# Kernel tuning notes

Hardware: AMD Instinct MI355X
Metric: run time of the kernel (lower is better)

The kernel has to match this reference:

```python
import jax, jax.numpy as jnp
import numpy as np

RC, RMIN = 6.0, 0.5
BETA, M1, M2 = 12, 24, 6
B, N, NT, MN = 4, 1024, 2, 128
K = NT * MN
NFEAT = M1 * M2


def _cheby(x, order):
    # Chebyshev polynomials T_0..T_{order-1} via recurrence, stacked on last axis
    Ts = [jnp.ones_like(x), x]
    for _ in range(order - 2):
        Ts.append(2.0 * x * Ts[-1] - Ts[-2])
    return jnp.stack(Ts[:order], axis=-1)


def _feat_fn(rxyz, valid, ti_map, c_param, scale):
    # rxyz: (B,N,K,3) neighbor displacement vectors; valid: (B,N,K) 0/1 float
    b, n, k, _ = rxyz.shape
    r = jnp.sqrt(jnp.sum(rxyz * rxyz, axis=-1) + 1e-12)          # (B,N,K)
    u = jnp.clip((r - RMIN) / (RC - RMIN), 0.0, 1.0)
    fc = 0.5 * (jnp.cos(jnp.pi * u) + 1.0) * valid                # smooth cutoff
    x = 2.0 * (r - RMIN) / (RC - RMIN) - 1.0
    T = _cheby(x, BETA).reshape(b, n, NT, MN, BETA)               # group slots by neighbor type
    c_i = c_param[ti_map]                                         # (N, NT, M1, BETA) gather by center type
    s = jnp.einsum('bntmk,ntfk->bntmf', T, c_i).reshape(b, n, k, M1)
    s = s * fc[..., None]                                         # (B,N,K,M1)
    inv_r = valid / r
    sr = jnp.concatenate([valid[..., None], rxyz * inv_r[..., None]], axis=-1)  # (B,N,K,4)
    R = jnp.einsum('bnkf,bnkc->bnfc', s, sr) / MN                 # (B,N,M1,4)
    feat = jnp.einsum('bnfc,bngc->bnfg', R, R[:, :, :M2]).reshape(b, n, NFEAT)
    return feat * scale


def _ei_fn(feat, ti_map, W0, b0, W1, b1, W2, b2, ener_shift):
    # evaluate all per-type fitting nets, then select by atom type
    h = jnp.tanh(jnp.einsum('bnf,tfh->bnth', feat, W0) + b0)
    h2 = jnp.tanh(jnp.einsum('bnth,thg->bntg', h, W1) + b1) + h   # resnet skip
    E = jnp.einsum('bnth,th->bnt', h2, W2) + b2 + ener_shift      # (B,N,T)
    idx = jnp.broadcast_to(ti_map[None, :, None], (E.shape[0], E.shape[1], 1))
    return jnp.take_along_axis(E, idx, axis=2)[..., 0]            # (B,N)


def setup_inputs() -> dict:
    key = jax.random.key(0)
    ks = jax.random.split(key, 16)
    num_neigh = jax.random.randint(ks[0], (B, N, NT), MN // 2, MN + 1)
    slot = jnp.arange(MN)
    vmask = slot[None, None, None, :] < num_neigh[..., None]      # (B,N,NT,MN)
    ln = jax.random.randint(ks[1], (B, N, NT, MN), 0, N)
    list_neigh = jnp.where(vmask, ln, -1)
    r = jax.random.uniform(ks[2], (B, N, K), minval=RMIN + 0.2, maxval=RC - 0.1)
    d = jax.random.normal(ks[3], (B, N, K, 3))
    d = d / jnp.linalg.norm(d, axis=-1, keepdims=True)
    rxyz = d * r[..., None]
    vm = vmask.reshape(B, N, K).astype(jnp.float32)
    ImageDR = jnp.concatenate([r[..., None], rxyz], axis=-1) * vm[..., None]
    return {
        'list_neigh': list_neigh,
        'Imagetype_map': jax.random.randint(ks[4], (N,), 0, NT),
        'atom_type': jnp.arange(NT),
        'ImageDR': ImageDR.astype(jnp.float32),
        'num_neigh': num_neigh,
        'nghost': 0,
        'c_param': jax.random.normal(ks[5], (NT, NT, M1, BETA), jnp.float32) * 0.3,
        'scale': jax.random.uniform(ks[6], (NFEAT,), jnp.float32, 0.5, 1.5),
        'W0': jax.random.normal(ks[7], (NT, NFEAT, 128), jnp.float32) * 0.08,
        'b0': jnp.zeros((NT, 128), jnp.float32),
        'W1': jax.random.normal(ks[8], (NT, 128, 128), jnp.float32) * 0.08,
        'b1': jnp.zeros((NT, 128), jnp.float32),
        'W2': jax.random.normal(ks[9], (NT, 128), jnp.float32) * 0.08,
        'b2': jnp.zeros((NT,), jnp.float32),
        'ener_shift': jax.random.normal(ks[10], (NT,), jnp.float32),
    }


def reference(list_neigh, Imagetype_map, atom_type, ImageDR, num_neigh, nghost,
              c_param, scale, W0, b0, W1, b1, W2, b2, ener_shift):
    ln = list_neigh.reshape(B, N, K)
    valid = (ln >= 0).astype(ImageDR.dtype)
    rxyz = ImageDR[..., 1:4]

    def etot(z):
        feat = _feat_fn(z, valid, Imagetype_map, c_param, scale)
        return _ei_fn(feat, Imagetype_map, W0, b0, W1, b1, W2, b2, ener_shift)

    Ei = etot(rxyz)                                               # (B,N)
    Etot = jnp.sum(Ei, axis=1)                                    # (B,)
    g = jax.grad(lambda z: etot(z).sum())(rxyz)                   # dE/dr_ij  (B,N,K,3)

    natom_tot = N + nghost
    Force = jnp.zeros((B, natom_tot, 3), ImageDR.dtype)
    Force = Force.at[:, :N].add(g.sum(axis=2))                    # center-atom contribution
    idx = jnp.where(ln >= 0, ln, natom_tot).reshape(B, N * K)     # invalid -> pad slot

    def scat(i, v):
        buf = jnp.zeros((natom_tot + 1, 3), v.dtype)
        return buf.at[i].add(v)[:natom_tot]

    Force = Force + jax.vmap(scat)(idx, (-g).reshape(B, N * K, 3))  # scatter to neighbors
    Virial = -jnp.einsum('bnkc,bnkd->bcd', rxyz, g).reshape(B, 9)
    return (Etot, Ei, Force, Virial)
```

## Files before the change

kernel.cpp:

```cpp
#include <hip/hip_runtime.h>
#include <math.h>

#define RMINF  0.5f
#define LSPAN  5.5f
constexpr int BETA = 12, M1 = 24, M2 = 6;
constexpr int B_ = 4, N_ = 1024, NT_ = 2, MN_ = 128;
constexpr int K_ = NT_ * MN_;
constexpr int NFEAT = M1 * M2;
constexpr int HID = 128;
constexpr float PI_F = 3.14159265358979323846f;

constexpr int EI_OFF = B_;
constexpr int F_OFF  = B_ + B_ * N_;
constexpr int V_OFF  = F_OFF + B_ * N_ * 3;

constexpr int G_ = 4;
constexpr int NG = B_ * N_ / G_;
constexpr int SL = 8;

constexpr size_t WS_FEAT    = 0;
constexpr size_t WS_R       = (size_t)B_ * N_ * NFEAT;
constexpr size_t WS_VIR     = WS_R + (size_t)B_ * N_ * 96;
constexpr size_t WS_CONTRIB = WS_VIR + (size_t)NG * 9;
constexpr size_t WS_PARTIAL = WS_CONTRIB + (size_t)NG * N_ * 3;


__global__ __launch_bounds__(256) void k1_embed(
    const int*   __restrict__ list_neigh,
    const int*   __restrict__ type_map,
    const float* __restrict__ imagedr,
    const float* __restrict__ c_param,
    const float* __restrict__ scale,
    float* __restrict__ feat_ws,
    float* __restrict__ R_ws)
{
    __shared__ float c_sh[NT_ * M1 * BETA];
    __shared__ float p_sh[K_][13];
    __shared__ float sr_sh[K_][5];
    __shared__ float Mpart[2][96];
    __shared__ float R_sh[96];

    const int tid = threadIdx.x;
    const int bn = blockIdx.x;
    const int n  = bn % N_;
    const int tn = type_map[n];

    for (int i = tid; i < NT_ * M1 * BETA; i += 256)
        c_sh[i] = c_param[tn * (NT_ * M1 * BETA) + i];

    const int k = tid;
    const int lni = list_neigh[(size_t)bn * K_ + k];
    const float valid = (lni >= 0) ? 1.0f : 0.0f;

    const float4 dr4 = reinterpret_cast<const float4*>(imagedr)[(size_t)bn * K_ + k];
    const float rx = dr4.y, ry = dr4.z, rz = dr4.w;
    const float r  = sqrtf(rx*rx + ry*ry + rz*rz + 1e-12f);
    const float uraw = (r - RMINF) / LSPAN;
    const float u  = fminf(fmaxf(uraw, 0.0f), 1.0f);
    const float fc = 0.5f * (cosf(PI_F * u) + 1.0f) * valid;
    const float x  = 2.0f * (r - RMINF) / LSPAN - 1.0f;

    float T[BETA];
    T[0] = 1.0f; T[1] = x;
#pragma unroll
    for (int j = 2; j < BETA; ++j) T[j] = 2.0f * x * T[j-1] - T[j-2];

    const float inv_r = 1.0f / r;
    sr_sh[k][0] = valid;
    sr_sh[k][1] = valid * rx * inv_r;
    sr_sh[k][2] = valid * ry * inv_r;
    sr_sh[k][3] = valid * rz * inv_r;
#pragma unroll
    for (int j = 0; j < BETA; ++j) p_sh[k][j] = fc * T[j];
    __syncthreads();

    if (tid < 192) {
        const int sub = tid / 96, idx = tid % 96;
        const int tk = idx / 48, rem = idx % 48;
        const int j = rem >> 2, cc = rem & 3;
        const int k0 = tk * 128 + sub * 64;
        float a0 = 0.0f, a1 = 0.0f;
        for (int kk = k0; kk < k0 + 64; kk += 2) {
            a0 = fmaf(p_sh[kk][j],   sr_sh[kk][cc],   a0);
            a1 = fmaf(p_sh[kk+1][j], sr_sh[kk+1][cc], a1);
        }
        Mpart[sub][idx] = a0 + a1;
    }
    __syncthreads();

    if (tid < 96) {
        const int f = tid >> 2, cc = tid & 3;
        float acc = 0.0f;
#pragma unroll
        for (int tk = 0; tk < NT_; ++tk) {
#pragma unroll
            for (int j = 0; j < BETA; ++j) {
                const float m = Mpart[0][tk*48 + j*4 + cc] + Mpart[1][tk*48 + j*4 + cc];
                acc = fmaf(c_sh[tk*288 + f*12 + j], m, acc);
            }
        }
        const float v = acc * (1.0f / MN_);
        R_sh[tid] = v;
        R_ws[(size_t)bn * 96 + tid] = v;
    }
    __syncthreads();
    if (tid < NFEAT) {
        const int f = tid / 6, g = tid % 6;
        float acc = 0.0f;
#pragma unroll
        for (int c = 0; c < 4; ++c) acc += R_sh[f * 4 + c] * R_sh[g * 4 + c];
        feat_ws[(size_t)bn * NFEAT + tid] = acc * scale[tid];
    }
}

__global__ __launch_bounds__(256) void k2_mlp(
    const int*   __restrict__ type_map,
    const float* __restrict__ scale,
    const float* __restrict__ W0,
    const float* __restrict__ b0,
    const float* __restrict__ W1,
    const float* __restrict__ b1,
    const float* __restrict__ W2,
    const float* __restrict__ b2,
    const float* __restrict__ eshift,
    const float* __restrict__ feat_ws,
    float* __restrict__ dfeat_ws,
    float* __restrict__ out)
{
    __shared__ float feat_sh[2][4][NFEAT];
    __shared__ float h_sh[2][4][HID];
    __shared__ float dz1_sh[2][4][HID];
    __shared__ float dz0_sh[2][4][HID];
    __shared__ float red[4][4];

    const int tid  = threadIdx.x;
    const int half = tid >> 7;
    const int c    = tid & 127;
    const int lane = tid & 63;
    const int wid  = tid >> 6;
    const int n0 = blockIdx.x * 2;
    const int n_h = n0 + half;
    const int tn = type_map[n_h];

    for (int i = tid; i < 8 * NFEAT; i += 256) {
        const int a = i / NFEAT, f = i % NFEAT;
        const int hh = a >> 2, bb = a & 3;
        feat_sh[hh][bb][f] = feat_ws[((size_t)bb * N_ + n0 + hh) * NFEAT + f];
    }
    __syncthreads();

    float acc[4];
    const float bias0 = b0[tn * HID + c];
#pragma unroll
    for (int b = 0; b < 4; ++b) acc[b] = bias0;
    const float* w0c = W0 + (size_t)tn * NFEAT * HID + c;
#pragma unroll 4
    for (int f = 0; f < NFEAT; ++f) {
        const float w = w0c[(size_t)f * HID];
#pragma unroll
        for (int b = 0; b < 4; ++b) acc[b] = fmaf(feat_sh[half][b][f], w, acc[b]);
    }
    float hv[4];
#pragma unroll
    for (int b = 0; b < 4; ++b) { hv[b] = tanhf(acc[b]); h_sh[half][b][c] = hv[b]; }
    __syncthreads();

    const float bias1 = b1[tn * HID + c];
#pragma unroll
    for (int b = 0; b < 4; ++b) acc[b] = bias1;
    const float* w1c = W1 + (size_t)tn * HID * HID + c;
#pragma unroll 4
    for (int g = 0; g < HID; ++g) {
        const float w = w1c[(size_t)g * HID];
#pragma unroll
        for (int b = 0; b < 4; ++b) acc[b] = fmaf(h_sh[half][b][g], w, acc[b]);
    }
    const float w2c = W2[tn * HID + c];
    float ei[4];
#pragma unroll
    for (int b = 0; b < 4; ++b) {
        const float t1 = tanhf(acc[b]);
        dz1_sh[half][b][c] = w2c * (1.0f - t1 * t1);
        ei[b] = (t1 + hv[b]) * w2c;
    }
#pragma unroll
    for (int b = 0; b < 4; ++b) {
        float v = ei[b];
#pragma unroll
        for (int m = 32; m >= 1; m >>= 1) v += __shfl_xor(v, m);
        if (lane == 0) red[wid][b] = v;
    }
    __syncthreads();
    if (tid < 8) {
        const int hh = tid >> 2, bb = tid & 3;
        const int nn = n0 + hh;
        const int tt = type_map[nn];
        out[EI_OFF + (size_t)bb * N_ + nn] =
            red[hh*2][bb] + red[hh*2+1][bb] + b2[tt] + eshift[tt];
    }

    {
        const float4* w1row = reinterpret_cast<const float4*>(W1 + (size_t)(tn * HID + c) * HID);
        float ar[4];
#pragma unroll
        for (int b = 0; b < 4; ++b) ar[b] = w2c;
#pragma unroll 2
        for (int g4 = 0; g4 < HID / 4; ++g4) {
            const float4 w = w1row[g4];
#pragma unroll
            for (int b = 0; b < 4; ++b) {
                ar[b] += w.x * dz1_sh[half][b][g4*4+0] + w.y * dz1_sh[half][b][g4*4+1]
                       + w.z * dz1_sh[half][b][g4*4+2] + w.w * dz1_sh[half][b][g4*4+3];
            }
        }
#pragma unroll
        for (int b = 0; b < 4; ++b) dz0_sh[half][b][c] = ar[b] * (1.0f - hv[b] * hv[b]);
    }
    __syncthreads();

    for (int f = c; f < NFEAT; f += HID) {
        const float4* w0row = reinterpret_cast<const float4*>(W0 + (size_t)(tn * NFEAT + f) * HID);
        float ar[4] = {0.0f, 0.0f, 0.0f, 0.0f};
#pragma unroll 2
        for (int h4 = 0; h4 < HID / 4; ++h4) {
            const float4 w = w0row[h4];
#pragma unroll
            for (int b = 0; b < 4; ++b) {
                ar[b] += w.x * dz0_sh[half][b][h4*4+0] + w.y * dz0_sh[half][b][h4*4+1]
                       + w.z * dz0_sh[half][b][h4*4+2] + w.w * dz0_sh[half][b][h4*4+3];
            }
        }
        const float sc = scale[f];
#pragma unroll
        for (int b = 0; b < 4; ++b)
            dfeat_ws[((size_t)b * N_ + n_h) * NFEAT + f] = ar[b] * sc;
    }
}

__global__ __launch_bounds__(256) void k3_bwd(
    const int*   __restrict__ list_neigh,
    const int*   __restrict__ type_map,
    const float* __restrict__ imagedr,
    const float* __restrict__ c_param,
    const float* __restrict__ dfeat_ws,
    const float* __restrict__ R_ws,
    float* __restrict__ contrib_ws,
    float* __restrict__ vir_ws)
{
    __shared__ float fcontrib[N_ * 3];
    __shared__ float c_sh[NT_ * M1 * BETA];
    __shared__ float dfeat_sh[NFEAT];
    __shared__ float R_sh[96];
    __shared__ float dR_sh[96];
    __shared__ float A_sh[96];
    __shared__ float red12[12 * 4];

    const int tid  = threadIdx.x;
    const int lane = tid & 63;
    const int wid  = tid >> 6;
    const int g  = blockIdx.x;
    const int tk = tid >> 7;

    for (int i = tid; i < N_ * 3; i += 256) fcontrib[i] = 0.0f;

    float vv0=0.f,vv1=0.f,vv2=0.f,vv3=0.f,vv4=0.f,vv5=0.f,vv6=0.f,vv7=0.f,vv8=0.f;

    for (int aa = 0; aa < G_; ++aa) {
        const int bn = g * G_ + aa;
        const int n  = bn & (N_ - 1);
        const int tn = type_map[n];

        __syncthreads();
        for (int i = tid; i < NT_ * M1 * BETA; i += 256)
            c_sh[i] = c_param[tn * (NT_ * M1 * BETA) + i];
        if (tid < NFEAT) dfeat_sh[tid] = dfeat_ws[(size_t)bn * NFEAT + tid];
        if (tid < 96)    R_sh[tid]     = R_ws[(size_t)bn * 96 + tid];
        __syncthreads();

        if (tid < 96) {
            const int p = tid >> 2, c = tid & 3;
            float acc = 0.0f;
#pragma unroll
            for (int gg = 0; gg < M2; ++gg) acc += dfeat_sh[p * 6 + gg] * R_sh[gg * 4 + c];
            if (p < M2) {
                for (int f = 0; f < M1; ++f) acc += dfeat_sh[f * 6 + p] * R_sh[f * 4 + c];
            }
            dR_sh[p * 4 + c] = acc * (1.0f / MN_);
        }
        __syncthreads();

        if (tid < 96) {
            const int atk = tid / 48, rem = tid % 48;
            const int j = rem >> 2, cc = rem & 3;
            float acc = 0.0f;
#pragma unroll
            for (int f = 0; f < M1; ++f)
                acc = fmaf(c_sh[atk*288 + f*12 + j], dR_sh[f*4 + cc], acc);
            A_sh[tid] = acc;
        }
        __syncthreads();

        const int lni = list_neigh[(size_t)bn * K_ + tid];
        const float valid = (lni >= 0) ? 1.0f : 0.0f;
        const float4 dr4 = reinterpret_cast<const float4*>(imagedr)[(size_t)bn * K_ + tid];
        const float rx = dr4.y, ry = dr4.z, rz = dr4.w;
        const float r  = sqrtf(rx*rx + ry*ry + rz*rz + 1e-12f);
        const float uraw = (r - RMINF) / LSPAN;
        const float u  = fminf(fmaxf(uraw, 0.0f), 1.0f);
        const float fc = 0.5f * (cosf(PI_F * u) + 1.0f) * valid;
        const float x  = 2.0f * (r - RMINF) / LSPAN - 1.0f;

        float T[BETA];
        T[0] = 1.0f; T[1] = x;
#pragma unroll
        for (int j = 2; j < BETA; ++j) T[j] = 2.0f * x * T[j-1] - T[j-2];

        const float inv_r = 1.0f / r;
        const float sr0 = valid;
        const float sr1 = valid * rx * inv_r;
        const float sr2 = valid * ry * inv_r;
        const float sr3 = valid * rz * inv_r;

        const float* Arow = &A_sh[tk * 48];
        float dfc = 0.0f, dx = 0.0f;
        float tA0 = 0.0f, tA1 = 0.0f, tA2 = 0.0f, tA3 = 0.0f;
        float tpm1 = 1.0f, tpm2 = 0.0f;
#pragma unroll
        for (int j = 0; j < BETA; ++j) {
            const float a0 = Arow[j*4+0], a1 = Arow[j*4+1];
            const float a2 = Arow[j*4+2], a3 = Arow[j*4+3];
            const float cjj = a0*sr0 + a1*sr1 + a2*sr2 + a3*sr3;
            dfc = fmaf(T[j], cjj, dfc);
            tA0 = fmaf(T[j], a0, tA0);
            tA1 = fmaf(T[j], a1, tA1);
            tA2 = fmaf(T[j], a2, tA2);
            tA3 = fmaf(T[j], a3, tA3);
            if (j == 1) {
                dx = cjj;
            } else if (j >= 2) {
                const float tp = 2.0f * T[j-1] + 2.0f * x * tpm1 - tpm2;
                dx = fmaf(cjj, tp, dx);
                tpm2 = tpm1; tpm1 = tp;
            }
        }
        const float dsr1 = fc * tA1, dsr2 = fc * tA2, dsr3 = fc * tA3;

        float dfcdr = 0.0f;
        if (uraw > 0.0f && uraw < 1.0f)
            dfcdr = -0.5f * PI_F * sinf(PI_F * u) * valid / LSPAN;
        const float drt = (fc * dx) * (2.0f / LSPAN) + dfc * dfcdr;
        const float Sdot = dsr1 * rx + dsr2 * ry + dsr3 * rz;
        const float common = drt * inv_r - valid * Sdot * inv_r * inv_r * inv_r;
        const float gx = common * rx + valid * dsr1 * inv_r;
        const float gy = common * ry + valid * dsr2 * inv_r;
        const float gz = common * rz + valid * dsr3 * inv_r;

        if (lni >= 0) {
            atomicAdd(&fcontrib[lni * 3 + 0], -gx);
            atomicAdd(&fcontrib[lni * 3 + 1], -gy);
            atomicAdd(&fcontrib[lni * 3 + 2], -gz);
        }

        {
            float s0 = gx, s1 = gy, s2 = gz;
#pragma unroll
            for (int m = 32; m >= 1; m >>= 1) {
                s0 += __shfl_xor(s0, m);
                s1 += __shfl_xor(s1, m);
                s2 += __shfl_xor(s2, m);
            }
            if (lane == 0) {
                red12[0 * 4 + wid] = s0;
                red12[1 * 4 + wid] = s1;
                red12[2 * 4 + wid] = s2;
            }
        }
        __syncthreads();
        if (tid < 3) {
            const float v = red12[tid*4+0] + red12[tid*4+1] + red12[tid*4+2] + red12[tid*4+3];
            atomicAdd(&fcontrib[n * 3 + tid], v);
        }

        vv0 = fmaf(-rx, gx, vv0); vv1 = fmaf(-rx, gy, vv1); vv2 = fmaf(-rx, gz, vv2);
        vv3 = fmaf(-ry, gx, vv3); vv4 = fmaf(-ry, gy, vv4); vv5 = fmaf(-ry, gz, vv5);
        vv6 = fmaf(-rz, gx, vv6); vv7 = fmaf(-rz, gy, vv7); vv8 = fmaf(-rz, gz, vv8);
    }

    {
        float vals[9] = {vv0,vv1,vv2,vv3,vv4,vv5,vv6,vv7,vv8};
        __syncthreads();
#pragma unroll
        for (int i = 0; i < 9; ++i) {
            float v = vals[i];
#pragma unroll
            for (int m = 32; m >= 1; m >>= 1) v += __shfl_xor(v, m);
            if (lane == 0) red12[i * 4 + wid] = v;
        }
        __syncthreads();
        if (tid < 9)
            vir_ws[(size_t)g * 9 + tid] = red12[tid*4+0] + red12[tid*4+1]
                                        + red12[tid*4+2] + red12[tid*4+3];
    }

    __syncthreads();
    {
        float4* dst = reinterpret_cast<float4*>(contrib_ws + (size_t)g * (N_ * 3));
        const float4* src = reinterpret_cast<const float4*>(fcontrib);
        for (int i = tid; i < (N_ * 3) / 4; i += 256) dst[i] = src[i];
    }
}

__global__ __launch_bounds__(256) void k3_reduce(
    const float* __restrict__ contrib_ws,
    float* __restrict__ partial_ws)
{
    const int x  = blockIdx.x;
    const int ch = x % 3;
    const int bb = (x / 3) % B_;
    const int s  = x / (3 * B_);
    const int c4 = ch * 256 + threadIdx.x;
    const int rows = (NG / B_) / SL;
    const int g0 = bb * (NG / B_) + s * rows;

    const float4* src = reinterpret_cast<const float4*>(contrib_ws);
    float4 a0 = {0,0,0,0}, a1 = {0,0,0,0};
    for (int r = 0; r < rows; r += 2) {
        const float4 v0 = src[(size_t)(g0 + r)     * 768 + c4];
        const float4 v1 = src[(size_t)(g0 + r + 1) * 768 + c4];
        a0.x += v0.x; a0.y += v0.y; a0.z += v0.z; a0.w += v0.w;
        a1.x += v1.x; a1.y += v1.y; a1.z += v1.z; a1.w += v1.w;
    }
    const float4 res = {a0.x + a1.x, a0.y + a1.y, a0.z + a1.z, a0.w + a1.w};
    reinterpret_cast<float4*>(partial_ws)[(size_t)(s * B_ + bb) * 768 + c4] = res;
}

__global__ __launch_bounds__(256) void k4_final(
    const float* __restrict__ vir_ws,
    const float* __restrict__ partial_ws,
    float* __restrict__ out)
{
    __shared__ float red[10 * 4];
    const int tid  = threadIdx.x;
    const int lane = tid & 63;
    const int wid  = tid >> 6;
    const int b = blockIdx.x;

    for (int i = tid; i < N_ * 3; i += 256) {
        float f = 0.0f;
#pragma unroll
        for (int s = 0; s < SL; ++s) f += partial_ws[(size_t)(s * B_ + b) * (N_ * 3) + i];
        out[F_OFF + (size_t)b * (N_ * 3) + i] = f;
    }

    float vals[10];
#pragma unroll
    for (int i = 0; i < 10; ++i) vals[i] = 0.0f;
    for (int n = tid; n < N_; n += 256) vals[0] += out[EI_OFF + b * N_ + n];
    {
        const float* vp = vir_ws + ((size_t)b * (NG / B_) + tid) * 9;
#pragma unroll
        for (int j = 0; j < 9; ++j) vals[1 + j] = vp[j];
    }
#pragma unroll
    for (int i = 0; i < 10; ++i) {
        float v = vals[i];
#pragma unroll
        for (int m = 32; m >= 1; m >>= 1) v += __shfl_xor(v, m);
        if (lane == 0) red[i * 4 + wid] = v;
    }
    __syncthreads();
    if (tid < 10) {
        const float v = red[tid*4+0] + red[tid*4+1] + red[tid*4+2] + red[tid*4+3];
        if (tid == 0) out[b] = v;
        else          out[V_OFF + b * 9 + (tid - 1)] = v;
    }
}

extern "C" void kernel_launch(void* const* d_in, const int* in_sizes, int n_in,
                              void* d_out, int out_size, void* d_ws, size_t ws_size,
                              hipStream_t stream) {
    float* out = (float*)d_out;
    float* ws  = (float*)d_ws;
    float* feat_ws    = ws + WS_FEAT;
    float* R_ws       = ws + WS_R;
    float* vir_ws     = ws + WS_VIR;
    float* contrib_ws = ws + WS_CONTRIB;
    float* partial_ws = ws + WS_PARTIAL;

    const int*   list_neigh = (const int*)d_in[0];
    const int*   type_map   = (const int*)d_in[1];
    const float* imagedr    = (const float*)d_in[3];
    const float* c_param    = (const float*)d_in[6];
    const float* scale      = (const float*)d_in[7];
    const float* W0 = (const float*)d_in[8];
    const float* b0 = (const float*)d_in[9];
    const float* W1 = (const float*)d_in[10];
    const float* b1 = (const float*)d_in[11];
    const float* W2 = (const float*)d_in[12];
    const float* b2 = (const float*)d_in[13];
    const float* eshift = (const float*)d_in[14];

    k1_embed<<<B_ * N_, 256, 0, stream>>>(list_neigh, type_map, imagedr, c_param,
                                          scale, feat_ws, R_ws);
    k2_mlp<<<N_ / 2, 256, 0, stream>>>(type_map, scale, W0, b0, W1, b1, W2, b2,
                                       eshift, feat_ws, feat_ws , out);
    k3_bwd<<<NG, 256, 0, stream>>>(list_neigh, type_map, imagedr, c_param,
                                   feat_ws , R_ws, contrib_ws, vir_ws);
    k3_reduce<<<SL * B_ * 3, 256, 0, stream>>>(contrib_ws, partial_ws);
    k4_final<<<B_, 256, 0, stream>>>(vir_ws, partial_ws, out);
}
```

Baseline: 194.4 us.

## Remap MLP kernel to one atom per block with one batch per thread slice

The fitting-net kernel now runs one block of 512 threads per atom, and each group of 128 threads handles one batch element. Before, a 256-thread block handled two atoms, with every thread looping over all four batches. This doubles the block count and cuts per-thread register work, at the cost of each weight load being reused across only one batch per thread rather than four. The backward dot products also split into two accumulators for more instruction-level parallelism.

```diff
diff --git a/kernel.cpp b/kernel.cpp
--- a/kernel.cpp
+++ b/kernel.cpp
@@ -113,7 +113,7 @@
     }
 }
 
-__global__ __launch_bounds__(256) void k2_mlp(
+__global__ __launch_bounds__(512) void k2_mlp(
     const int*   __restrict__ type_map,
     const float* __restrict__ scale,
     const float* __restrict__ W0,
@@ -127,113 +127,84 @@
     float* __restrict__ dfeat_ws,
     float* __restrict__ out)
 {
-    __shared__ float feat_sh[2][4][NFEAT];
-    __shared__ float h_sh[2][4][HID];
-    __shared__ float dz1_sh[2][4][HID];
-    __shared__ float dz0_sh[2][4][HID];
-    __shared__ float red[4][4];
+    __shared__ float feat_sh[4][NFEAT];
+    __shared__ float h_sh[4][HID];
+    __shared__ float dz1_sh[4][HID];
+    __shared__ float dz0_sh[4][HID];
+    __shared__ float red[8];
 
     const int tid  = threadIdx.x;
-    const int half = tid >> 7;
+    const int b    = tid >> 7;
     const int c    = tid & 127;
     const int lane = tid & 63;
     const int wid  = tid >> 6;
-    const int n0 = blockIdx.x * 2;
-    const int n_h = n0 + half;
-    const int tn = type_map[n_h];
-
-    for (int i = tid; i < 8 * NFEAT; i += 256) {
-        const int a = i / NFEAT, f = i % NFEAT;
-        const int hh = a >> 2, bb = a & 3;
-        feat_sh[hh][bb][f] = feat_ws[((size_t)bb * N_ + n0 + hh) * NFEAT + f];
-    }
-    __syncthreads();
-
-    float acc[4];
-    const float bias0 = b0[tn * HID + c];
-#pragma unroll
-    for (int b = 0; b < 4; ++b) acc[b] = bias0;
+    const int n  = blockIdx.x;
+    const int tn = type_map[n];
+
+    for (int i = tid; i < 4 * NFEAT; i += 512) {
+        const int bb = i / NFEAT, f = i % NFEAT;
+        feat_sh[bb][f] = feat_ws[((size_t)bb * N_ + n) * NFEAT + f];
+    }
+    __syncthreads();
+
+    float acc = b0[tn * HID + c];
     const float* w0c = W0 + (size_t)tn * NFEAT * HID + c;
-#pragma unroll 4
-    for (int f = 0; f < NFEAT; ++f) {
-        const float w = w0c[(size_t)f * HID];
-#pragma unroll
-        for (int b = 0; b < 4; ++b) acc[b] = fmaf(feat_sh[half][b][f], w, acc[b]);
-    }
-    float hv[4];
-#pragma unroll
-    for (int b = 0; b < 4; ++b) { hv[b] = tanhf(acc[b]); h_sh[half][b][c] = hv[b]; }
-    __syncthreads();
-
-    const float bias1 = b1[tn * HID + c];
-#pragma unroll
-    for (int b = 0; b < 4; ++b) acc[b] = bias1;
+#pragma unroll 8
+    for (int f = 0; f < NFEAT; ++f)
+        acc = fmaf(feat_sh[b][f], w0c[(size_t)f * HID], acc);
+    const float h = tanhf(acc);
+    h_sh[b][c] = h;
+    __syncthreads();
+
+    float acc1 = b1[tn * HID + c];
     const float* w1c = W1 + (size_t)tn * HID * HID + c;
-#pragma unroll 4
-    for (int g = 0; g < HID; ++g) {
-        const float w = w1c[(size_t)g * HID];
-#pragma unroll
-        for (int b = 0; b < 4; ++b) acc[b] = fmaf(h_sh[half][b][g], w, acc[b]);
-    }
+#pragma unroll 8
+    for (int g = 0; g < HID; ++g)
+        acc1 = fmaf(h_sh[b][g], w1c[(size_t)g * HID], acc1);
+    const float t1 = tanhf(acc1);
     const float w2c = W2[tn * HID + c];
-    float ei[4];
-#pragma unroll
-    for (int b = 0; b < 4; ++b) {
-        const float t1 = tanhf(acc[b]);
-        dz1_sh[half][b][c] = w2c * (1.0f - t1 * t1);
-        ei[b] = (t1 + hv[b]) * w2c;
-    }
-#pragma unroll
-    for (int b = 0; b < 4; ++b) {
-        float v = ei[b];
+    dz1_sh[b][c] = w2c * (1.0f - t1 * t1);
+
+    {
+        float v = (t1 + h) * w2c;
 #pragma unroll
         for (int m = 32; m >= 1; m >>= 1) v += __shfl_xor(v, m);
-        if (lane == 0) red[wid][b] = v;
-    }
-    __syncthreads();
-    if (tid < 8) {
-        const int hh = tid >> 2, bb = tid & 3;
-        const int nn = n0 + hh;
-        const int tt = type_map[nn];
-        out[EI_OFF + (size_t)bb * N_ + nn] =
-            red[hh*2][bb] + red[hh*2+1][bb] + b2[tt] + eshift[tt];
-    }
+        if (lane == 0) red[wid] = v;
+    }
+    __syncthreads();
+    if (tid < 4)
+        out[EI_OFF + (size_t)tid * N_ + n] =
+            red[tid * 2] + red[tid * 2 + 1] + b2[tn] + eshift[tn];
 
     {
         const float4* w1row = reinterpret_cast<const float4*>(W1 + (size_t)(tn * HID + c) * HID);
-        float ar[4];
-#pragma unroll
-        for (int b = 0; b < 4; ++b) ar[b] = w2c;
-#pragma unroll 2
-        for (int g4 = 0; g4 < HID / 4; ++g4) {
-            const float4 w = w1row[g4];
-#pragma unroll
-            for (int b = 0; b < 4; ++b) {
-                ar[b] += w.x * dz1_sh[half][b][g4*4+0] + w.y * dz1_sh[half][b][g4*4+1]
-                       + w.z * dz1_sh[half][b][g4*4+2] + w.w * dz1_sh[half][b][g4*4+3];
-            }
-        }
-#pragma unroll
-        for (int b = 0; b < 4; ++b) dz0_sh[half][b][c] = ar[b] * (1.0f - hv[b] * hv[b]);
+        float ar = w2c, arb = 0.0f;
+#pragma unroll 4
+        for (int g4 = 0; g4 < HID / 4; g4 += 2) {
+            const float4 w  = w1row[g4];
+            const float4 w2 = w1row[g4 + 1];
+            ar  += w.x  * dz1_sh[b][g4*4+0] + w.y  * dz1_sh[b][g4*4+1]
+                 + w.z  * dz1_sh[b][g4*4+2] + w.w  * dz1_sh[b][g4*4+3];
+            arb += w2.x * dz1_sh[b][g4*4+4] + w2.y * dz1_sh[b][g4*4+5]
+                 + w2.z * dz1_sh[b][g4*4+6] + w2.w * dz1_sh[b][g4*4+7];
+        }
+        dz0_sh[b][c] = (ar + arb) * (1.0f - h * h);
     }
     __syncthreads();
 
     for (int f = c; f < NFEAT; f += HID) {
         const float4* w0row = reinterpret_cast<const float4*>(W0 + (size_t)(tn * NFEAT + f) * HID);
-        float ar[4] = {0.0f, 0.0f, 0.0f, 0.0f};
-#pragma unroll 2
-        for (int h4 = 0; h4 < HID / 4; ++h4) {
-            const float4 w = w0row[h4];
-#pragma unroll
-            for (int b = 0; b < 4; ++b) {
-                ar[b] += w.x * dz0_sh[half][b][h4*4+0] + w.y * dz0_sh[half][b][h4*4+1]
-                       + w.z * dz0_sh[half][b][h4*4+2] + w.w * dz0_sh[half][b][h4*4+3];
-            }
-        }
-        const float sc = scale[f];
-#pragma unroll
-        for (int b = 0; b < 4; ++b)
-            dfeat_ws[((size_t)b * N_ + n_h) * NFEAT + f] = ar[b] * sc;
+        float ar = 0.0f, arb = 0.0f;
+#pragma unroll 4
+        for (int h4 = 0; h4 < HID / 4; h4 += 2) {
+            const float4 w  = w0row[h4];
+            const float4 w2 = w0row[h4 + 1];
+            ar  += w.x  * dz0_sh[b][h4*4+0] + w.y  * dz0_sh[b][h4*4+1]
+                 + w.z  * dz0_sh[b][h4*4+2] + w.w  * dz0_sh[b][h4*4+3];
+            arb += w2.x * dz0_sh[b][h4*4+4] + w2.y * dz0_sh[b][h4*4+5]
+                 + w2.z * dz0_sh[b][h4*4+6] + w2.w * dz0_sh[b][h4*4+7];
+        }
+        dfeat_ws[((size_t)b * N_ + n) * NFEAT + f] = (ar + arb) * scale[f];
     }
 }
 
@@ -502,8 +473,8 @@
 
     k1_embed<<<B_ * N_, 256, 0, stream>>>(list_neigh, type_map, imagedr, c_param,
                                           scale, feat_ws, R_ws);
-    k2_mlp<<<N_ / 2, 256, 0, stream>>>(type_map, scale, W0, b0, W1, b1, W2, b2,
-                                       eshift, feat_ws, feat_ws , out);
+    k2_mlp<<<N_, 512, 0, stream>>>(type_map, scale, W0, b0, W1, b1, W2, b2,
+                                   eshift, feat_ws, feat_ws , out);
     k3_bwd<<<NG, 256, 0, stream>>>(list_neigh, type_map, imagedr, c_param,
                                    feat_ws , R_ws, contrib_ws, vir_ws);
     k3_reduce<<<SL * B_ * 3, 256, 0, stream>>>(contrib_ws, partial_ws);
```

After: 234.6 us. +20.7%, slower.
